# Performance work log

Hardware: AMD Instinct MI355X
Metric: run time of the kernel (lower is better)

The kernel has to match this reference:

```python
import jax, jax.numpy as jnp
import numpy as np

N = 100000      # nodes
E = 1250000     # edges
D_IN = 64
D_OUT = 64


def _gconv(x, src, dst, W_rel, W_root, b, n_nodes):
    # PyG GraphConv (aggr='add'): out = lin_rel(sum_{j in N(i)} x_j) + lin_root(x_i)
    agg = jax.ops.segment_sum(x[src], dst, num_segments=n_nodes)  # [N, d]
    return agg @ W_rel + b + x @ W_root


def setup_inputs() -> dict:
    key = jax.random.key(0)
    ks = jax.random.split(key, 12)
    graph = jax.random.normal(ks[0], (N, D_IN), dtype=jnp.float32)
    edge_index = jax.random.randint(ks[1], (2, E), 0, N, dtype=jnp.int32)
    s_in = 1.0 / np.sqrt(D_IN)
    s_out = 1.0 / np.sqrt(D_OUT)
    d = {
        "graph": graph,
        "edge_index": edge_index,
        "W1_rel": jax.random.uniform(ks[2], (D_IN, D_OUT), jnp.float32, -s_in, s_in),
        "W1_root": jax.random.uniform(ks[3], (D_IN, D_OUT), jnp.float32, -s_in, s_in),
        "b1": jnp.zeros((D_OUT,), jnp.float32),
        "W2_rel": jax.random.uniform(ks[4], (D_OUT, D_OUT), jnp.float32, -s_out, s_out),
        "W2_root": jax.random.uniform(ks[5], (D_OUT, D_OUT), jnp.float32, -s_out, s_out),
        "b2": jnp.zeros((D_OUT,), jnp.float32),
        "W3_rel": jax.random.uniform(ks[6], (D_OUT, D_OUT), jnp.float32, -s_out, s_out),
        "W3_root": jax.random.uniform(ks[7], (D_OUT, D_OUT), jnp.float32, -s_out, s_out),
        "b3": jnp.zeros((D_OUT,), jnp.float32),
    }
    return d


def reference(graph, edge_index, W1_rel, W1_root, b1, W2_rel, W2_root, b2, W3_rel, W3_root, b3):
    src, dst = edge_index[0], edge_index[1]
    n = graph.shape[0]
    y1 = jax.nn.elu(_gconv(graph, src, dst, W1_rel, W1_root, b1, n))
    y2 = jax.nn.elu(_gconv(y1, src, dst, W2_rel, W2_root, b2, n))
    y3 = jax.nn.sigmoid(_gconv(y2, src, dst, W3_rel, W3_root, b3, n))
    return (y1, y2, y3)
```

## Files before the change

### kernel.cpp

```cpp
#include <hip/hip_runtime.h>
#include <hip/hip_bf16.h>
#include <math.h>


#define D 64
#define BSHIFT 9
#define BW 512
#define BCAP 8192

typedef __attribute__((ext_vector_type(8))) short short8;
typedef __attribute__((ext_vector_type(4))) float f32x4;

__device__ __forceinline__ ushort f2b(float f) {
    uint x = __float_as_uint(f);
    uint r = (x + 0x7fffu + ((x >> 16) & 1u)) >> 16;
    return (ushort)r;
}
__device__ __forceinline__ float b2f(ushort u) {
    return __uint_as_float(((uint)u) << 16);
}


__global__ __launch_bounds__(256) void convert_w(const float* __restrict__ w0,
                                                 const float* __restrict__ w1,
                                                 const float* __restrict__ w2,
                                                 const float* __restrict__ w3,
                                                 const float* __restrict__ w4,
                                                 const float* __restrict__ w5,
                                                 ushort* __restrict__ out) {
    int m = blockIdx.x >> 4;
    int t = (blockIdx.x & 15) * 256 + threadIdx.x;
    const float* src = m == 0 ? w0 : m == 1 ? w1 : m == 2 ? w2 : m == 3 ? w3 : m == 4 ? w4 : w5;
    int k = t >> 6, d = t & 63;
    out[m * 4096 + d * 64 + k] = f2b(src[t]);
}


__global__ __launch_bounds__(1024) void bucket_scatter(const int* __restrict__ src,
                                                       const int* __restrict__ dst,
                                                       int* __restrict__ bucketCnt,
                                                       unsigned long long* __restrict__ store,
                                                       int E) {
    __shared__ int h[256], base[256], cur[256];
    int t = threadIdx.x;
    if (t < 256) { h[t] = 0; cur[t] = 0; }
    __syncthreads();
    int e = blockIdx.x * 1024 + t;
    int s = 0, d = 0, b = 0;
    bool ok = e < E;
    if (ok) {
        s = src[e];
        d = dst[e];
        b = d >> BSHIFT;
        atomicAdd(&h[b], 1);
    }
    __syncthreads();
    if (t < 256) base[t] = h[t] ? atomicAdd(&bucketCnt[t], h[t]) : 0;
    __syncthreads();
    if (ok) {
        int r = atomicAdd(&cur[b], 1);
        int pos = base[b] + r;
        if (pos < BCAP)
            store[(size_t)b * BCAP + pos] = ((unsigned long long)(uint)d << 32) | (uint)s;
    }
}


__global__ __launch_bounds__(256) void scan_buckets(const int* __restrict__ bucketCnt,
                                                    int* __restrict__ bucketBase,
                                                    int* __restrict__ offs,
                                                    int nb, int n, int E) {
    __shared__ int tmp[256];
    int t = threadIdx.x;
    int v = (t < nb) ? bucketCnt[t] : 0;
    tmp[t] = v;
    __syncthreads();
    for (int off = 1; off < 256; off <<= 1) {
        int add = (t >= off) ? tmp[t - off] : 0;
        __syncthreads();
        tmp[t] += add;
        __syncthreads();
    }
    if (t < nb) bucketBase[t] = tmp[t] - v;
    if (t == 0) offs[n] = E;
}


__global__ __launch_bounds__(1024) void bucket_build(const int* __restrict__ bucketCnt,
                                                     const int* __restrict__ bucketBase,
                                                     const unsigned long long* __restrict__ store,
                                                     int* __restrict__ offs,
                                                     int* __restrict__ src_sorted, int n) {
    __shared__ int h[BW], loc[BW], cur[BW];
    __shared__ unsigned long long se[BCAP];
    int b = blockIdx.x, t = threadIdx.x;
    int cnt = bucketCnt[b];
    if (cnt > BCAP) cnt = BCAP;
    int obase = bucketBase[b];
    int d0 = b << BSHIFT;
    int nd = n - d0;
    if (nd > BW) nd = BW;
    if (t < BW) { h[t] = 0; cur[t] = 0; }
    __syncthreads();
    for (int i = t; i < cnt; i += 1024) {
        unsigned long long p = store[(size_t)b * BCAP + i];
        se[i] = p;
        atomicAdd(&h[(int)(p >> 32) - d0], 1);
    }
    __syncthreads();
    if (t < BW) loc[t] = h[t];
    __syncthreads();
    for (int off = 1; off < BW; off <<= 1) {
        int add = (t < BW && t >= off) ? loc[t - off] : 0;
        __syncthreads();
        if (t < BW) loc[t] += add;
        __syncthreads();
    }
    if (t < nd) offs[d0 + t] = obase + loc[t] - h[t];
    __syncthreads();
    for (int i = t; i < cnt; i += 1024) {
        unsigned long long p = se[i];
        int dl = (int)(p >> 32) - d0;
        int r = atomicAdd(&cur[dl], 1);
        src_sorted[obase + loc[dl] - h[dl] + r] = (int)(p & 0xffffffffULL);
    }
}


__global__ __launch_bounds__(256) void gemm_ro(const float* __restrict__ x,
                                               const ushort* __restrict__ WtR,
                                               const ushort* __restrict__ WtO,
                                               const float* __restrict__ bias,
                                               ushort* __restrict__ hrel,
                                               ushort* __restrict__ hroot, int n) {
    __shared__ ushort hsR[4][16 * 64];
    __shared__ ushort hsO[4][16 * 64];
    int t = threadIdx.x;
    int w = t >> 6, l = t & 63;
    int i0 = blockIdx.x * 64 + w * 16;
    int lr = l & 15, kb = l >> 4;
    int row = i0 + lr;
    int rowc = row < n ? row : n - 1;

    short8 a[2];
#pragma unroll
    for (int s = 0; s < 2; ++s) {
        const float* p = x + (size_t)rowc * D + s * 32 + kb * 8;
        float4 u = *(const float4*)p;
        float4 v = *(const float4*)(p + 4);
        a[s][0] = f2b(u.x); a[s][1] = f2b(u.y); a[s][2] = f2b(u.z); a[s][3] = f2b(u.w);
        a[s][4] = f2b(v.x); a[s][5] = f2b(v.y); a[s][6] = f2b(v.z); a[s][7] = f2b(v.w);
    }

#pragma unroll
    for (int ct = 0; ct < 4; ++ct) {
        f32x4 accR = (f32x4){0.f, 0.f, 0.f, 0.f};
        f32x4 accO = (f32x4){0.f, 0.f, 0.f, 0.f};
#pragma unroll
        for (int s = 0; s < 2; ++s) {
            short8 bR = *(const short8*)(WtR + (ct * 16 + lr) * D + s * 32 + kb * 8);
            short8 bO = *(const short8*)(WtO + (ct * 16 + lr) * D + s * 32 + kb * 8);
            accR = __builtin_amdgcn_mfma_f32_16x16x32_bf16(a[s], bR, accR, 0, 0, 0);
            accO = __builtin_amdgcn_mfma_f32_16x16x32_bf16(a[s], bO, accO, 0, 0, 0);
        }
        float bv = bias[ct * 16 + lr];
#pragma unroll
        for (int i = 0; i < 4; ++i) {
            hsR[w][(kb * 4 + i) * 64 + ct * 16 + lr] = f2b(accR[i]);
            hsO[w][(kb * 4 + i) * 64 + ct * 16 + lr] = f2b(accO[i] + bv);
        }
    }
    __syncthreads();

    int r = l >> 2, ch = l & 3;
    int grow = i0 + r;
    if (grow < n) {
        const ushort* spR = &hsR[w][r * 64 + ch * 16];
        const ushort* spO = &hsO[w][r * 64 + ch * 16];
        float4 r0 = *(const float4*)spR;
        float4 r1 = *(const float4*)(spR + 8);
        float4 o0 = *(const float4*)spO;
        float4 o1 = *(const float4*)(spO + 8);
        *(float4*)(hrel + (size_t)grow * D + ch * 16) = r0;
        *(float4*)(hrel + (size_t)grow * D + ch * 16 + 8) = r1;
        *(float4*)(hroot + (size_t)grow * D + ch * 16) = o0;
        *(float4*)(hroot + (size_t)grow * D + ch * 16 + 8) = o1;
    }
}


template <int ACT>
__global__ __launch_bounds__(256) void agg_act(const ushort* __restrict__ hrel,
                                               const ushort* __restrict__ hroot,
                                               const int* __restrict__ offs,
                                               const int* __restrict__ srcs,
                                               float* __restrict__ y, int n) {
    int node = blockIdx.x * 4 + (threadIdx.x >> 6);
    int l = threadIdx.x & 63;
    if (node >= n) return;
    int q = l >> 4, r = l & 15;
    int beg = offs[node];
    int end = offs[node + 1];

    float a0 = 0.f, a1 = 0.f, a2 = 0.f, a3 = 0.f;
    for (int e0 = beg; e0 < end; e0 += 16) {
#pragma unroll
        for (int k = 0; k < 4; ++k) {
            int ee = e0 + k * 4 + q;
            int eec = ee < end ? ee : end - 1;
            int s = srcs[eec];
            uint2 u = *(const uint2*)(hrel + (size_t)s * D + r * 4);
            float m = (ee < end) ? 1.f : 0.f;
            a0 = fmaf(__uint_as_float(u.x << 16), m, a0);
            a1 = fmaf(__uint_as_float(u.x & 0xffff0000u), m, a1);
            a2 = fmaf(__uint_as_float(u.y << 16), m, a2);
            a3 = fmaf(__uint_as_float(u.y & 0xffff0000u), m, a3);
        }
    }

    a0 += __shfl_xor(a0, 32); a0 += __shfl_xor(a0, 16);
    a1 += __shfl_xor(a1, 32); a1 += __shfl_xor(a1, 16);
    a2 += __shfl_xor(a2, 32); a2 += __shfl_xor(a2, 16);
    a3 += __shfl_xor(a3, 32); a3 += __shfl_xor(a3, 16);

    uint2 hr = *(const uint2*)(hroot + (size_t)node * D + r * 4);
    a0 += __uint_as_float(hr.x << 16);
    a1 += __uint_as_float(hr.x & 0xffff0000u);
    a2 += __uint_as_float(hr.y << 16);
    a3 += __uint_as_float(hr.y & 0xffff0000u);

    if (ACT == 0) {
        a0 = a0 > 0.f ? a0 : expf(a0) - 1.f;
        a1 = a1 > 0.f ? a1 : expf(a1) - 1.f;
        a2 = a2 > 0.f ? a2 : expf(a2) - 1.f;
        a3 = a3 > 0.f ? a3 : expf(a3) - 1.f;
    } else {
        a0 = 1.f / (1.f + expf(-a0));
        a1 = 1.f / (1.f + expf(-a1));
        a2 = 1.f / (1.f + expf(-a2));
        a3 = 1.f / (1.f + expf(-a3));
    }

    if (q == 0) {
        float4 o; o.x = a0; o.y = a1; o.z = a2; o.w = a3;
        *(float4*)(y + (size_t)node * D + r * 4) = o;
    }
}


extern "C" void kernel_launch(void* const* d_in, const int* in_sizes, int n_in,
                              void* d_out, int out_size, void* d_ws, size_t ws_size,
                              hipStream_t stream) {
    const float* graph = (const float*)d_in[0];
    const int* eidx    = (const int*)d_in[1];
    const float* W1r = (const float*)d_in[2];
    const float* W1o = (const float*)d_in[3];
    const float* b1  = (const float*)d_in[4];
    const float* W2r = (const float*)d_in[5];
    const float* W2o = (const float*)d_in[6];
    const float* b2  = (const float*)d_in[7];
    const float* W3r = (const float*)d_in[8];
    const float* W3o = (const float*)d_in[9];
    const float* b3  = (const float*)d_in[10];

    int n = in_sizes[0] / D;
    int E = in_sizes[1] / 2;
    const int* src  = eidx;
    const int* dstl = eidx + E;
    int nb = (n + BW - 1) >> BSHIFT;

    char* w = (char*)d_ws;
    auto carve = [&](size_t bytes) {
        void* p = (void*)w;
        w += (bytes + 255) & ~(size_t)255;
        return p;
    };
    ushort* hrel  = (ushort*)carve((size_t)n * D * sizeof(ushort));
    ushort* hroot = (ushort*)carve((size_t)n * D * sizeof(ushort));
    unsigned long long* store = (unsigned long long*)hrel;
    int* offs       = (int*)carve((size_t)(n + 1) * sizeof(int));
    int* src_sorted = (int*)carve((size_t)E * sizeof(int));
    int* bucketCnt  = (int*)carve(256 * sizeof(int));
    int* bucketBase = (int*)carve(256 * sizeof(int));
    ushort* wt      = (ushort*)carve(6 * 4096 * sizeof(ushort));
    ushort* wtR1 = wt;
    ushort* wtO1 = wt + 1 * 4096;
    ushort* wtR2 = wt + 2 * 4096;
    ushort* wtO2 = wt + 3 * 4096;
    ushort* wtR3 = wt + 4 * 4096;
    ushort* wtO3 = wt + 5 * 4096;

    int eb1 = (E + 1023) / 1024;
    int tb  = (n + 63) / 64;
    int ab  = (n + 3) / 4;

    hipMemsetAsync(bucketCnt, 0, 256 * sizeof(int), stream);
    convert_w<<<96, 256, 0, stream>>>(W1r, W1o, W2r, W2o, W3r, W3o, wt);
    bucket_scatter<<<eb1, 1024, 0, stream>>>(src, dstl, bucketCnt, store, E);
    scan_buckets<<<1, 256, 0, stream>>>(bucketCnt, bucketBase, offs, nb, n, E);
    bucket_build<<<nb, 1024, 0, stream>>>(bucketCnt, bucketBase, store, offs, src_sorted, n);

    float* out = (float*)d_out;
    float* y1 = out;
    float* y2 = out + (size_t)n * D;
    float* y3 = out + 2 * (size_t)n * D;

    gemm_ro<<<tb, 256, 0, stream>>>(graph, wtR1, wtO1, b1, hrel, hroot, n);
    agg_act<0><<<ab, 256, 0, stream>>>(hrel, hroot, offs, src_sorted, y1, n);
    gemm_ro<<<tb, 256, 0, stream>>>(y1, wtR2, wtO2, b2, hrel, hroot, n);
    agg_act<0><<<ab, 256, 0, stream>>>(hrel, hroot, offs, src_sorted, y2, n);
    gemm_ro<<<tb, 256, 0, stream>>>(y2, wtR3, wtO3, b3, hrel, hroot, n);
    agg_act<1><<<ab, 256, 0, stream>>>(hrel, hroot, offs, src_sorted, y3, n);
}
```

Baseline: 328.8 us.

## Fold bucket-count zeroing into weight conversion and use fast exp/rcp

Removes the separate memset launch by zeroing the bucket counters inside the weight-conversion kernel. The activation epilogues switch to fast-math __expf and hardware reciprocal, and the LDS readback in the GEMM is rewritten with float4 pointer indexing. This saves one launch and some transcendental cost, at the price of slightly lower accuracy in the activations.

```diff
diff --git a/kernel.cpp b/kernel.cpp
--- a/kernel.cpp
+++ b/kernel.cpp
@@ -27,7 +27,9 @@
                                                  const float* __restrict__ w3,
                                                  const float* __restrict__ w4,
                                                  const float* __restrict__ w5,
-                                                 ushort* __restrict__ out) {
+                                                 ushort* __restrict__ out,
+                                                 int* __restrict__ bucketCnt) {
+    if (blockIdx.x == 0 && threadIdx.x < 256) bucketCnt[threadIdx.x] = 0;
     int m = blockIdx.x >> 4;
     int t = (blockIdx.x & 15) * 256 + threadIdx.x;
     const float* src = m == 0 ? w0 : m == 1 ? w1 : m == 2 ? w2 : m == 3 ? w3 : m == 4 ? w4 : w5;
@@ -175,12 +177,12 @@
     int r = l >> 2, ch = l & 3;
     int grow = i0 + r;
     if (grow < n) {
-        const ushort* spR = &hsR[w][r * 64 + ch * 16];
-        const ushort* spO = &hsO[w][r * 64 + ch * 16];
-        float4 r0 = *(const float4*)spR;
-        float4 r1 = *(const float4*)(spR + 8);
-        float4 o0 = *(const float4*)spO;
-        float4 o1 = *(const float4*)(spO + 8);
+        const float4* spR = (const float4*)&hsR[w][r * 64 + ch * 16];
+        const float4* spO = (const float4*)&hsO[w][r * 64 + ch * 16];
+        float4 r0 = spR[0];
+        float4 r1 = spR[1];
+        float4 o0 = spO[0];
+        float4 o1 = spO[1];
         *(float4*)(hrel + (size_t)grow * D + ch * 16) = r0;
         *(float4*)(hrel + (size_t)grow * D + ch * 16 + 8) = r1;
         *(float4*)(hroot + (size_t)grow * D + ch * 16) = o0;
@@ -230,15 +232,15 @@
     a3 += __uint_as_float(hr.y & 0xffff0000u);
 
     if (ACT == 0) {
-        a0 = a0 > 0.f ? a0 : expf(a0) - 1.f;
-        a1 = a1 > 0.f ? a1 : expf(a1) - 1.f;
-        a2 = a2 > 0.f ? a2 : expf(a2) - 1.f;
-        a3 = a3 > 0.f ? a3 : expf(a3) - 1.f;
+        a0 = a0 > 0.f ? a0 : __expf(a0) - 1.f;
+        a1 = a1 > 0.f ? a1 : __expf(a1) - 1.f;
+        a2 = a2 > 0.f ? a2 : __expf(a2) - 1.f;
+        a3 = a3 > 0.f ? a3 : __expf(a3) - 1.f;
     } else {
-        a0 = 1.f / (1.f + expf(-a0));
-        a1 = 1.f / (1.f + expf(-a1));
-        a2 = 1.f / (1.f + expf(-a2));
-        a3 = 1.f / (1.f + expf(-a3));
+        a0 = __builtin_amdgcn_rcpf(1.f + __expf(-a0));
+        a1 = __builtin_amdgcn_rcpf(1.f + __expf(-a1));
+        a2 = __builtin_amdgcn_rcpf(1.f + __expf(-a2));
+        a3 = __builtin_amdgcn_rcpf(1.f + __expf(-a3));
     }
 
     if (q == 0) {
@@ -294,8 +296,7 @@
     int tb  = (n + 63) / 64;
     int ab  = (n + 3) / 4;
 
-    hipMemsetAsync(bucketCnt, 0, 256 * sizeof(int), stream);
-    convert_w<<<96, 256, 0, stream>>>(W1r, W1o, W2r, W2o, W3r, W3o, wt);
+    convert_w<<<96, 256, 0, stream>>>(W1r, W1o, W2r, W2o, W3r, W3o, wt, bucketCnt);
     bucket_scatter<<<eb1, 1024, 0, stream>>>(src, dstl, bucketCnt, store, E);
     scan_buckets<<<1, 256, 0, stream>>>(bucketCnt, bucketBase, offs, nb, n, E);
     bucket_build<<<nb, 1024, 0, stream>>>(bucketCnt, bucketBase, store, offs, src_sorted, n);
```

Result: faster. 315.1 us (-4.2%).
